# Performance work log

Measured on AMD Instinct MI355X. Metric: run time of the kernel, lower is better.

Reference implementation:

```python
import jax, jax.numpy as jnp
import numpy as np

N_EMBD = 32
BLOCK = 8
N_HEADS = 4
HEAD = N_EMBD // N_HEADS  # 8


def setup_inputs() -> dict:
    key = jax.random.key(0)
    k_x, k_attn, k_proj, k_f1, k_f2 = jax.random.split(key, 5)
    b = 262144
    X = jax.random.normal(k_x, (b, BLOCK, N_EMBD), dtype=jnp.float32)
    # per-head fused qkv weight, stored (in, out) so y = x @ W; out = 3*HEAD, split K,Q,V
    W_attn = jax.random.normal(k_attn, (N_HEADS, N_EMBD, 3 * HEAD), dtype=jnp.float32) * 0.02
    W_proj = jax.random.normal(k_proj, (N_EMBD, N_EMBD), dtype=jnp.float32) * 0.02
    W_ff1 = jax.random.normal(k_f1, (N_EMBD, 4 * N_EMBD), dtype=jnp.float32) * 0.02
    W_ff2 = jax.random.normal(k_f2, (4 * N_EMBD, N_EMBD), dtype=jnp.float32) * 0.02
    return {"X": X, "W_attn": W_attn, "W_proj": W_proj, "W_ff1": W_ff1, "W_ff2": W_ff2}


def reference(X, W_attn, W_proj, W_ff1, W_ff2):
    b, t, c = X.shape
    # fused per-head QKV: (b, t, c) x (h, c, 3*HEAD) -> (b, h, t, 3*HEAD)
    qkv = jnp.einsum('btc,hcd->bhtd', X, W_attn)
    k, q, v = jnp.split(qkv, 3, axis=-1)  # split order K, Q, V as in torch .split
    # NOTE: scale uses full embed dim c, not head_size (faithful to source)
    scores = jnp.einsum('bhqd,bhkd->bhqk', q, k) * (c ** -0.5)
    causal = jnp.tril(jnp.ones((t, t), dtype=bool))
    scores = jnp.where(causal, scores, -jnp.inf)
    w = jax.nn.softmax(scores, axis=-1)
    attn = jnp.einsum('bhqk,bhkd->bhqd', w, v)  # (b, h, t, HEAD)
    attn = attn.transpose(0, 2, 1, 3).reshape(b, t, c)  # concat heads
    X = X + attn @ W_proj
    X = X + jax.nn.relu(X @ W_ff1) @ W_ff2
    return X
```

## Files before the change

kernel.cpp:

```cpp
#include <hip/hip_runtime.h>


typedef __attribute__((ext_vector_type(8))) short        bf16x8;
typedef __attribute__((ext_vector_type(4))) float        f32x4;
typedef __attribute__((ext_vector_type(4))) int          i32x4;
typedef __attribute__((ext_vector_type(2))) unsigned int u32x2;

#define THREADS 256
#define TPB 64
#define TPW 16

#define LDS_X     0
#define LDS_QK    1280
#define LDS_VT    3584
#define LDS_P2    5120
#define LDS_ATTN  0
#define LDS_X2    1280
#define LDS_HID   2560
#define LDS_OUT   0
#define LDS_WAVE  7680

__device__ __forceinline__ unsigned pk_bf16(float a, float b) {
    unsigned r;
    asm("v_cvt_pk_bf16_f32 %0, %1, %2" : "=v"(r) : "v"(a), "v"(b));
    return r;
}

union frag_u { i32x4 i; bf16x8 b; };

__device__ __forceinline__ bf16x8 gather_w(const float* p, int ldk, int g) {
    frag_u r;
    #pragma unroll
    for (int jj = 0; jj < 4; ++jj) {
        float a = p[(8 * g + 2 * jj) * ldk];
        float b = p[(8 * g + 2 * jj + 1) * ldk];
        r.i[jj] = (int)pk_bf16(a, b);
    }
    return r.b;
}

__global__ __launch_bounds__(THREADS)
void block_mfma(const float* __restrict__ X,
                const float* __restrict__ Wattn,
                const float* __restrict__ Wproj,
                const float* __restrict__ Wff1,
                const float* __restrict__ Wff2,
                float* __restrict__ Out,
                int ntiles)
{
    __shared__ __align__(16) char smem[4 * LDS_WAVE];

    const int lane = threadIdx.x & 63;
    const int wid  = threadIdx.x >> 6;
    const int g    = lane >> 4;
    const int c    = lane & 15;
    char* W = smem + wid * LDS_WAVE;

    const float scale = 0.17677669529663687f;
    const f32x4 z4 = {0.f, 0.f, 0.f, 0.f};

    bf16x8 wqk[4], wv[2], wp[2], w1[8], w2[2][4];
    #pragma unroll
    for (int n = 0; n < 4; ++n)
        wqk[n] = gather_w(Wattn + n * 768 + c, 24, g);
    #pragma unroll
    for (int n = 0; n < 2; ++n) {
        int vch = 16 * n + c;
        wv[n] = gather_w(Wattn + (vch >> 3) * 768 + 16 + (vch & 7), 24, g);
    }
    #pragma unroll
    for (int n = 0; n < 2; ++n)
        wp[n] = gather_w(Wproj + 16 * n + c, 32, g);
    #pragma unroll
    for (int n = 0; n < 8; ++n)
        w1[n] = gather_w(Wff1 + 16 * n + c, 128, g);
    #pragma unroll
    for (int n = 0; n < 2; ++n)
        #pragma unroll
        for (int ks = 0; ks < 4; ++ks)
            w2[n][ks] = gather_w(Wff2 + ks * 1024 + 16 * n + c, 32, g);

    float mf[4];
    #pragma unroll
    for (int r = 0; r < 4; ++r) {
        int key = 4 * g + r;
        mf[r] = ((key >> 3) == (c >> 3) && (key & 7) <= (c & 7)) ? 1.f : 0.f;
    }
    const int mQK = (lane < 16) ? -1 : 0;
    const int mA  = (((lane >> 3) & 1) == ((lane >> 5) & 1)) ? -1 : 0;
    const i32x4 vQK = {mQK, mQK, mQK, mQK};
    const i32x4 vA  = {mA, mA, mA, mA};

    const int tile0 = blockIdx.x * TPB + wid * TPW;

    const float* xg0 = X + (size_t)tile0 * 512;
    f32x4 xa = *(const f32x4*)(xg0 + lane * 8);
    f32x4 xb = *(const f32x4*)(xg0 + lane * 8 + 4);

    #pragma unroll 1
    for (int it = 0; it < TPW; ++it) {
        const int tile = tile0 + it;
        if (tile >= ntiles) break;
        const float* xgc = X + (size_t)tile * 512;
        float* outg = Out + (size_t)tile * 512;

        f32x4 rx0 = *(const f32x4*)(xgc + c * 32 + 4 * g);
        f32x4 rx1 = *(const f32x4*)(xgc + c * 32 + 16 + 4 * g);

        {
            i32x4 xi = { (int)pk_bf16(xa[0], xa[1]), (int)pk_bf16(xa[2], xa[3]),
                         (int)pk_bf16(xb[0], xb[1]), (int)pk_bf16(xb[2], xb[3]) };
            *(i32x4*)(void*)(W + LDS_X + (lane >> 2) * 80 + (lane & 3) * 16) = xi;
        }

        {
            const int tn = (it + 1 < TPW && tile + 1 < ntiles) ? tile + 1 : tile;
            const float* xgn = X + (size_t)tn * 512;
            xa = *(const f32x4*)(xgn + lane * 8);
            xb = *(const f32x4*)(xgn + lane * 8 + 4);
        }

        frag_u xf; xf.i = *(i32x4*)(void*)(W + LDS_X + c * 80 + g * 16);

        #pragma unroll
        for (int n = 0; n < 4; ++n) {
            f32x4 qc = __builtin_amdgcn_mfma_f32_16x16x32_bf16(wqk[n], xf.b, z4, 0, 0, 0);
            u32x2 w64 = { pk_bf16(qc[0], qc[1]), pk_bf16(qc[2], qc[3]) };
            *(u32x2*)(void*)(W + LDS_QK + c * 144 + (16 * n + 4 * g) * 2) = w64;
        }
        #pragma unroll
        for (int n = 0; n < 2; ++n) {
            f32x4 vc = __builtin_amdgcn_mfma_f32_16x16x32_bf16(xf.b, wv[n], z4, 0, 0, 0);
            u32x2 w64 = { pk_bf16(vc[0], vc[1]), pk_bf16(vc[2], vc[3]) };
            *(u32x2*)(void*)(W + LDS_VT + (16 * n + c) * 48 + 4 * g * 2) = w64;
        }

        #pragma unroll
        for (int h = 0; h < 4; ++h) {
            frag_u kf, qf;
            kf.i = *(i32x4*)(void*)(W + LDS_QK + c * 144 + 32 * h);
            qf.i = *(i32x4*)(void*)(W + LDS_QK + c * 144 + 32 * h + 16);
            kf.i &= vQK; qf.i &= vQK;
            f32x4 sT = __builtin_amdgcn_mfma_f32_16x16x32_bf16(kf.b, qf.b, z4, 0, 0, 0);
            float e0 = __expf(sT[0] * scale) * mf[0];
            float e1 = __expf(sT[1] * scale) * mf[1];
            float e2 = __expf(sT[2] * scale) * mf[2];
            float e3 = __expf(sT[3] * scale) * mf[3];
            float s = (e0 + e1) + (e2 + e3);
            s += __shfl_xor(s, 16);
            s += __shfl_xor(s, 32);
            float rs = 1.0f / s;
            u32x2 w64 = { pk_bf16(e0 * rs, e1 * rs), pk_bf16(e2 * rs, e3 * rs) };
            *(u32x2*)(void*)(W + LDS_P2 + (h >> 1) * 1280 + c * 80 + ((h & 1) * 16 + 4 * g) * 2) = w64;
        }

        #pragma unroll
        for (int p = 0; p < 2; ++p) {
            frag_u va, pb;
            va.i = *(i32x4*)(void*)(W + LDS_VT + (16 * p + c) * 48 + (g & 1) * 16);
            va.i &= vA;
            pb.i = *(i32x4*)(void*)(W + LDS_P2 + p * 1280 + c * 80 + g * 16);
            f32x4 pv = __builtin_amdgcn_mfma_f32_16x16x32_bf16(va.b, pb.b, z4, 0, 0, 0);
            u32x2 w64 = { pk_bf16(pv[0], pv[1]), pk_bf16(pv[2], pv[3]) };
            *(u32x2*)(void*)(W + LDS_ATTN + c * 80 + (16 * p + 4 * g) * 2) = w64;
        }

        frag_u af; af.i = *(i32x4*)(void*)(W + LDS_ATTN + c * 80 + g * 16);
        f32x4 x2c[2];
        #pragma unroll
        for (int n = 0; n < 2; ++n) {
            f32x4 pc = __builtin_amdgcn_mfma_f32_16x16x32_bf16(wp[n], af.b, z4, 0, 0, 0);
            f32x4 rx = (n == 0) ? rx0 : rx1;
            #pragma unroll
            for (int r = 0; r < 4; ++r) x2c[n][r] = pc[r] + rx[r];
            u32x2 w64 = { pk_bf16(x2c[n][0], x2c[n][1]), pk_bf16(x2c[n][2], x2c[n][3]) };
            *(u32x2*)(void*)(W + LDS_X2 + c * 80 + (16 * n + 4 * g) * 2) = w64;
        }

        frag_u bf; bf.i = *(i32x4*)(void*)(W + LDS_X2 + c * 80 + g * 16);
        #pragma unroll
        for (int n = 0; n < 8; ++n) {
            f32x4 hc = __builtin_amdgcn_mfma_f32_16x16x32_bf16(w1[n], bf.b, z4, 0, 0, 0);
            #pragma unroll
            for (int r = 0; r < 4; ++r) hc[r] = fmaxf(hc[r], 0.f);
            u32x2 w64 = { pk_bf16(hc[0], hc[1]), pk_bf16(hc[2], hc[3]) };
            *(u32x2*)(void*)(W + LDS_HID + c * 272 + (16 * n + 4 * g) * 2) = w64;
        }

        frag_u hf0, hf1, hf2, hf3;
        hf0.i = *(i32x4*)(void*)(W + LDS_HID + c * 272 + 0 * 64 + g * 16);
        hf1.i = *(i32x4*)(void*)(W + LDS_HID + c * 272 + 1 * 64 + g * 16);
        hf2.i = *(i32x4*)(void*)(W + LDS_HID + c * 272 + 2 * 64 + g * 16);
        hf3.i = *(i32x4*)(void*)(W + LDS_HID + c * 272 + 3 * 64 + g * 16);
        #pragma unroll
        for (int n = 0; n < 2; ++n) {
            f32x4 oc = x2c[n];
            oc = __builtin_amdgcn_mfma_f32_16x16x32_bf16(w2[n][0], hf0.b, oc, 0, 0, 0);
            oc = __builtin_amdgcn_mfma_f32_16x16x32_bf16(w2[n][1], hf1.b, oc, 0, 0, 0);
            oc = __builtin_amdgcn_mfma_f32_16x16x32_bf16(w2[n][2], hf2.b, oc, 0, 0, 0);
            oc = __builtin_amdgcn_mfma_f32_16x16x32_bf16(w2[n][3], hf3.b, oc, 0, 0, 0);
            *(f32x4*)(void*)(W + LDS_OUT + c * 144 + (16 * n + 4 * g) * 4) = oc;
        }

        f32x4 r0 = *(f32x4*)(void*)(W + LDS_OUT + (lane >> 2) * 144 + (lane & 3) * 32);
        f32x4 r1 = *(f32x4*)(void*)(W + LDS_OUT + (lane >> 2) * 144 + (lane & 3) * 32 + 16);
        *(f32x4*)(outg + lane * 8)     = r0;
        *(f32x4*)(outg + lane * 8 + 4) = r1;
    }
}

extern "C" void kernel_launch(void* const* d_in, const int* in_sizes, int n_in,
                              void* d_out, int out_size, void* d_ws, size_t ws_size,
                              hipStream_t stream) {
    (void)n_in; (void)out_size; (void)d_ws; (void)ws_size;
    const float* X     = (const float*)d_in[0];
    const float* Wattn = (const float*)d_in[1];
    const float* Wproj = (const float*)d_in[2];
    const float* Wff1  = (const float*)d_in[3];
    const float* Wff2  = (const float*)d_in[4];
    float* Out = (float*)d_out;

    const int nseq   = in_sizes[0] / 256;
    const int ntiles = nseq / 2;
    const int blocks = (ntiles + TPB - 1) / TPB;
    block_mfma<<<dim3(blocks), dim3(THREADS), 0, stream>>>(
        X, Wattn, Wproj, Wff1, Wff2, Out, ntiles);
}
```

Before: 214.2 us.

## Interleave two tiles per wave iteration with double LDS contexts and fold softmax scale

Each wave now processes two tiles per loop iteration in separate LDS contexts, running each phase on tile A and then tile B. The intent is to give the scheduler independent MFMA and LDS work so it can hide dependency latencies within a single wave. The softmax scale and log2(e) factor are folded into the Q/K weights so scores feed exp2 directly, and the reciprocal uses the hardware rcp. The hidden-buffer row stride changes from 272 to 304 bytes, presumably to reduce LDS bank conflicts. Costs are doubled LDS per block (lower occupancy) and higher register pressure, plus slight precision changes from rcp and from scaling the weights before the bf16 conversion.

```diff
diff --git a/kernel.cpp b/kernel.cpp
--- a/kernel.cpp
+++ b/kernel.cpp
@@ -18,7 +18,7 @@
 #define LDS_X2    1280
 #define LDS_HID   2560
 #define LDS_OUT   0
-#define LDS_WAVE  7680
+#define LDS_CTX   7680
 
 __device__ __forceinline__ unsigned pk_bf16(float a, float b) {
     unsigned r;
@@ -28,16 +28,132 @@
 
 union frag_u { i32x4 i; bf16x8 b; };
 
-__device__ __forceinline__ bf16x8 gather_w(const float* p, int ldk, int g) {
+__device__ __forceinline__ bf16x8 gather_w(const float* p, int ldk, int g, float s) {
     frag_u r;
     #pragma unroll
     for (int jj = 0; jj < 4; ++jj) {
-        float a = p[(8 * g + 2 * jj) * ldk];
-        float b = p[(8 * g + 2 * jj + 1) * ldk];
+        float a = p[(8 * g + 2 * jj) * ldk] * s;
+        float b = p[(8 * g + 2 * jj + 1) * ldk] * s;
         r.i[jj] = (int)pk_bf16(a, b);
     }
     return r.b;
 }
+
+
+__device__ __forceinline__ void ph_stage(char* Wc, int lane, const f32x4& xa, const f32x4& xb) {
+    i32x4 xi = { (int)pk_bf16(xa[0], xa[1]), (int)pk_bf16(xa[2], xa[3]),
+                 (int)pk_bf16(xb[0], xb[1]), (int)pk_bf16(xb[2], xb[3]) };
+    *(i32x4*)(void*)(Wc + LDS_X + (lane >> 2) * 80 + (lane & 3) * 16) = xi;
+}
+
+__device__ __forceinline__ void ph_qkv(char* Wc, int c, int g,
+                                       const bf16x8 (&wqk)[4], const bf16x8 (&wv)[2]) {
+    const f32x4 z4 = {0.f, 0.f, 0.f, 0.f};
+    frag_u xf; xf.i = *(i32x4*)(void*)(Wc + LDS_X + c * 80 + g * 16);
+    #pragma unroll
+    for (int n = 0; n < 4; ++n) {
+        f32x4 qc = __builtin_amdgcn_mfma_f32_16x16x32_bf16(wqk[n], xf.b, z4, 0, 0, 0);
+        u32x2 w64 = { pk_bf16(qc[0], qc[1]), pk_bf16(qc[2], qc[3]) };
+        *(u32x2*)(void*)(Wc + LDS_QK + c * 144 + (16 * n + 4 * g) * 2) = w64;
+    }
+    #pragma unroll
+    for (int n = 0; n < 2; ++n) {
+        f32x4 vc = __builtin_amdgcn_mfma_f32_16x16x32_bf16(xf.b, wv[n], z4, 0, 0, 0);
+        u32x2 w64 = { pk_bf16(vc[0], vc[1]), pk_bf16(vc[2], vc[3]) };
+        *(u32x2*)(void*)(Wc + LDS_VT + (16 * n + c) * 48 + 8 * g) = w64;
+    }
+}
+
+__device__ __forceinline__ void ph_scores(char* Wc, int c, int g,
+                                          const f32x4& mf, const i32x4& mQK) {
+    const f32x4 z4 = {0.f, 0.f, 0.f, 0.f};
+    #pragma unroll
+    for (int h = 0; h < 4; ++h) {
+        frag_u kf, qf;
+        kf.i = *(i32x4*)(void*)(Wc + LDS_QK + c * 144 + 32 * h);
+        qf.i = *(i32x4*)(void*)(Wc + LDS_QK + c * 144 + 32 * h + 16);
+        kf.i &= mQK; qf.i &= mQK;
+        f32x4 sT = __builtin_amdgcn_mfma_f32_16x16x32_bf16(kf.b, qf.b, z4, 0, 0, 0);
+        float e0 = __builtin_amdgcn_exp2f(sT[0]) * mf[0];
+        float e1 = __builtin_amdgcn_exp2f(sT[1]) * mf[1];
+        float e2 = __builtin_amdgcn_exp2f(sT[2]) * mf[2];
+        float e3 = __builtin_amdgcn_exp2f(sT[3]) * mf[3];
+        float s = (e0 + e1) + (e2 + e3);
+        s += __shfl_xor(s, 16);
+        s += __shfl_xor(s, 32);
+        float rs = __builtin_amdgcn_rcpf(s);
+        u32x2 w64 = { pk_bf16(e0 * rs, e1 * rs), pk_bf16(e2 * rs, e3 * rs) };
+        *(u32x2*)(void*)(Wc + LDS_P2 + (h >> 1) * 1280 + c * 80 + ((h & 1) * 16 + 4 * g) * 2) = w64;
+    }
+}
+
+__device__ __forceinline__ void ph_pv(char* Wc, int c, int g, const i32x4& mPV) {
+    const f32x4 z4 = {0.f, 0.f, 0.f, 0.f};
+    #pragma unroll
+    for (int p = 0; p < 2; ++p) {
+        frag_u va, pb;
+        va.i = *(i32x4*)(void*)(Wc + LDS_VT + (16 * p + c) * 48 + (g & 1) * 16);
+        va.i &= mPV;
+        pb.i = *(i32x4*)(void*)(Wc + LDS_P2 + p * 1280 + c * 80 + g * 16);
+        f32x4 pv = __builtin_amdgcn_mfma_f32_16x16x32_bf16(va.b, pb.b, z4, 0, 0, 0);
+        u32x2 w64 = { pk_bf16(pv[0], pv[1]), pk_bf16(pv[2], pv[3]) };
+        *(u32x2*)(void*)(Wc + LDS_ATTN + c * 80 + (16 * p + 4 * g) * 2) = w64;
+    }
+}
+
+__device__ __forceinline__ void ph_proj(char* Wc, int c, int g, const bf16x8 (&wp)[2],
+                                        const f32x4& rx0, const f32x4& rx1, f32x4 (&x2c)[2]) {
+    frag_u af; af.i = *(i32x4*)(void*)(Wc + LDS_ATTN + c * 80 + g * 16);
+    #pragma unroll
+    for (int n = 0; n < 2; ++n) {
+        const f32x4 z4 = {0.f, 0.f, 0.f, 0.f};
+        f32x4 pc = __builtin_amdgcn_mfma_f32_16x16x32_bf16(wp[n], af.b, z4, 0, 0, 0);
+        f32x4 rx = (n == 0) ? rx0 : rx1;
+        #pragma unroll
+        for (int r = 0; r < 4; ++r) x2c[n][r] = pc[r] + rx[r];
+        u32x2 w64 = { pk_bf16(x2c[n][0], x2c[n][1]), pk_bf16(x2c[n][2], x2c[n][3]) };
+        *(u32x2*)(void*)(Wc + LDS_X2 + c * 80 + (16 * n + 4 * g) * 2) = w64;
+    }
+}
+
+__device__ __forceinline__ void ph_ff1(char* Wc, int c, int g, const bf16x8 (&w1)[8]) {
+    frag_u bf; bf.i = *(i32x4*)(void*)(Wc + LDS_X2 + c * 80 + g * 16);
+    #pragma unroll
+    for (int n = 0; n < 8; ++n) {
+        const f32x4 z4 = {0.f, 0.f, 0.f, 0.f};
+        f32x4 hc = __builtin_amdgcn_mfma_f32_16x16x32_bf16(w1[n], bf.b, z4, 0, 0, 0);
+        #pragma unroll
+        for (int r = 0; r < 4; ++r) hc[r] = fmaxf(hc[r], 0.f);
+        u32x2 w64 = { pk_bf16(hc[0], hc[1]), pk_bf16(hc[2], hc[3]) };
+        *(u32x2*)(void*)(Wc + LDS_HID + c * 304 + (16 * n + 4 * g) * 2) = w64;
+    }
+}
+
+__device__ __forceinline__ void ph_ff2(char* Wc, int c, int g,
+                                       const bf16x8 (&w2)[2][4], const f32x4 (&x2c)[2]) {
+    frag_u hf0, hf1, hf2, hf3;
+    hf0.i = *(i32x4*)(void*)(Wc + LDS_HID + c * 304 + 0 * 64 + g * 16);
+    hf1.i = *(i32x4*)(void*)(Wc + LDS_HID + c * 304 + 1 * 64 + g * 16);
+    hf2.i = *(i32x4*)(void*)(Wc + LDS_HID + c * 304 + 2 * 64 + g * 16);
+    hf3.i = *(i32x4*)(void*)(Wc + LDS_HID + c * 304 + 3 * 64 + g * 16);
+    #pragma unroll
+    for (int n = 0; n < 2; ++n) {
+        f32x4 oc = x2c[n];
+        oc = __builtin_amdgcn_mfma_f32_16x16x32_bf16(w2[n][0], hf0.b, oc, 0, 0, 0);
+        oc = __builtin_amdgcn_mfma_f32_16x16x32_bf16(w2[n][1], hf1.b, oc, 0, 0, 0);
+        oc = __builtin_amdgcn_mfma_f32_16x16x32_bf16(w2[n][2], hf2.b, oc, 0, 0, 0);
+        oc = __builtin_amdgcn_mfma_f32_16x16x32_bf16(w2[n][3], hf3.b, oc, 0, 0, 0);
+        *(f32x4*)(void*)(Wc + LDS_OUT + c * 144 + (16 * n + 4 * g) * 4) = oc;
+    }
+}
+
+__device__ __forceinline__ void ph_store(char* Wc, int lane, float* outg) {
+    f32x4 r0 = *(f32x4*)(void*)(Wc + LDS_OUT + (lane >> 2) * 144 + (lane & 3) * 32);
+    f32x4 r1 = *(f32x4*)(void*)(Wc + LDS_OUT + (lane >> 2) * 144 + (lane & 3) * 32 + 16);
+    *(f32x4*)(outg + lane * 8)     = r0;
+    *(f32x4*)(outg + lane * 8 + 4) = r1;
+}
+
 
 __global__ __launch_bounds__(THREADS)
 void block_mfma(const float* __restrict__ X,
@@ -48,164 +164,105 @@
                 float* __restrict__ Out,
                 int ntiles)
 {
-    __shared__ __align__(16) char smem[4 * LDS_WAVE];
+    __shared__ __align__(16) char smem[4 * 2 * LDS_CTX];
 
     const int lane = threadIdx.x & 63;
     const int wid  = threadIdx.x >> 6;
     const int g    = lane >> 4;
     const int c    = lane & 15;
-    char* W = smem + wid * LDS_WAVE;
-
-    const float scale = 0.17677669529663687f;
-    const f32x4 z4 = {0.f, 0.f, 0.f, 0.f};
+    char* WA = smem + wid * (2 * LDS_CTX);
+    char* WB = WA + LDS_CTX;
+
+    const float wscale = 0.5050098f;
 
     bf16x8 wqk[4], wv[2], wp[2], w1[8], w2[2][4];
     #pragma unroll
     for (int n = 0; n < 4; ++n)
-        wqk[n] = gather_w(Wattn + n * 768 + c, 24, g);
+        wqk[n] = gather_w(Wattn + n * 768 + c, 24, g, wscale);
     #pragma unroll
     for (int n = 0; n < 2; ++n) {
         int vch = 16 * n + c;
-        wv[n] = gather_w(Wattn + (vch >> 3) * 768 + 16 + (vch & 7), 24, g);
+        wv[n] = gather_w(Wattn + (vch >> 3) * 768 + 16 + (vch & 7), 24, g, 1.f);
     }
     #pragma unroll
     for (int n = 0; n < 2; ++n)
-        wp[n] = gather_w(Wproj + 16 * n + c, 32, g);
+        wp[n] = gather_w(Wproj + 16 * n + c, 32, g, 1.f);
     #pragma unroll
     for (int n = 0; n < 8; ++n)
-        w1[n] = gather_w(Wff1 + 16 * n + c, 128, g);
+        w1[n] = gather_w(Wff1 + 16 * n + c, 128, g, 1.f);
     #pragma unroll
     for (int n = 0; n < 2; ++n)
         #pragma unroll
         for (int ks = 0; ks < 4; ++ks)
-            w2[n][ks] = gather_w(Wff2 + ks * 1024 + 16 * n + c, 32, g);
-
-    float mf[4];
+            w2[n][ks] = gather_w(Wff2 + ks * 1024 + 16 * n + c, 32, g, 1.f);
+
+    f32x4 mf;
     #pragma unroll
     for (int r = 0; r < 4; ++r) {
         int key = 4 * g + r;
         mf[r] = ((key >> 3) == (c >> 3) && (key & 7) <= (c & 7)) ? 1.f : 0.f;
     }
-    const int mQK = (lane < 16) ? -1 : 0;
-    const int mA  = (((lane >> 3) & 1) == ((lane >> 5) & 1)) ? -1 : 0;
-    const i32x4 vQK = {mQK, mQK, mQK, mQK};
-    const i32x4 vA  = {mA, mA, mA, mA};
+    const int b0 = (lane < 16) ? -1 : 0;
+    const int b1 = (((lane >> 3) & 1) == ((lane >> 5) & 1)) ? -1 : 0;
+    const i32x4 mQK = {b0, b0, b0, b0};
+    const i32x4 mPV = {b1, b1, b1, b1};
 
     const int tile0 = blockIdx.x * TPB + wid * TPW;
-
-    const float* xg0 = X + (size_t)tile0 * 512;
-    f32x4 xa = *(const f32x4*)(xg0 + lane * 8);
-    f32x4 xb = *(const f32x4*)(xg0 + lane * 8 + 4);
+    if (tile0 >= ntiles) return;
+
+    int p0 = tile0, p1 = (tile0 + 1 < ntiles) ? tile0 + 1 : ntiles - 1;
+    f32x4 xaA = *(const f32x4*)(X + (size_t)p0 * 512 + lane * 8);
+    f32x4 xbA = *(const f32x4*)(X + (size_t)p0 * 512 + lane * 8 + 4);
+    f32x4 xaB = *(const f32x4*)(X + (size_t)p1 * 512 + lane * 8);
+    f32x4 xbB = *(const f32x4*)(X + (size_t)p1 * 512 + lane * 8 + 4);
 
     #pragma unroll 1
-    for (int it = 0; it < TPW; ++it) {
-        const int tile = tile0 + it;
-        if (tile >= ntiles) break;
-        const float* xgc = X + (size_t)tile * 512;
-        float* outg = Out + (size_t)tile * 512;
-
-        f32x4 rx0 = *(const f32x4*)(xgc + c * 32 + 4 * g);
-        f32x4 rx1 = *(const f32x4*)(xgc + c * 32 + 16 + 4 * g);
+    for (int it = 0; it < TPW; it += 2) {
+        const int iA = tile0 + it;
+        const int iB = tile0 + it + 1;
+        const int ttA = (iA < ntiles) ? iA : ntiles - 1;
+        const int ttB = (iB < ntiles) ? iB : ntiles - 1;
+        const float* xgA = X + (size_t)ttA * 512;
+        const float* xgB = X + (size_t)ttB * 512;
+
+        f32x4 rxA0 = *(const f32x4*)(xgA + c * 32 + 4 * g);
+        f32x4 rxA1 = *(const f32x4*)(xgA + c * 32 + 16 + 4 * g);
+        f32x4 rxB0 = *(const f32x4*)(xgB + c * 32 + 4 * g);
+        f32x4 rxB1 = *(const f32x4*)(xgB + c * 32 + 16 + 4 * g);
+
+        ph_stage(WA, lane, xaA, xbA);
+        ph_stage(WB, lane, xaB, xbB);
 
         {
-            i32x4 xi = { (int)pk_bf16(xa[0], xa[1]), (int)pk_bf16(xa[2], xa[3]),
-                         (int)pk_bf16(xb[0], xb[1]), (int)pk_bf16(xb[2], xb[3]) };
-            *(i32x4*)(void*)(W + LDS_X + (lane >> 2) * 80 + (lane & 3) * 16) = xi;
+            int nA = (it + 2 < TPW && iA + 2 < ntiles) ? iA + 2 : ttA;
+            int nB = (it + 3 < TPW && iB + 2 < ntiles) ? iB + 2 : ttB;
+            xaA = *(const f32x4*)(X + (size_t)nA * 512 + lane * 8);
+            xbA = *(const f32x4*)(X + (size_t)nA * 512 + lane * 8 + 4);
+            xaB = *(const f32x4*)(X + (size_t)nB * 512 + lane * 8);
+            xbB = *(const f32x4*)(X + (size_t)nB * 512 + lane * 8 + 4);
         }
 
-        {
-            const int tn = (it + 1 < TPW && tile + 1 < ntiles) ? tile + 1 : tile;
-            const float* xgn = X + (size_t)tn * 512;
-            xa = *(const f32x4*)(xgn + lane * 8);
-            xb = *(const f32x4*)(xgn + lane * 8 + 4);
-        }
-
-        frag_u xf; xf.i = *(i32x4*)(void*)(W + LDS_X + c * 80 + g * 16);
-
-        #pragma unroll
-        for (int n = 0; n < 4; ++n) {
-            f32x4 qc = __builtin_amdgcn_mfma_f32_16x16x32_bf16(wqk[n], xf.b, z4, 0, 0, 0);
-            u32x2 w64 = { pk_bf16(qc[0], qc[1]), pk_bf16(qc[2], qc[3]) };
-            *(u32x2*)(void*)(W + LDS_QK + c * 144 + (16 * n + 4 * g) * 2) = w64;
-        }
-        #pragma unroll
-        for (int n = 0; n < 2; ++n) {
-            f32x4 vc = __builtin_amdgcn_mfma_f32_16x16x32_bf16(xf.b, wv[n], z4, 0, 0, 0);
-            u32x2 w64 = { pk_bf16(vc[0], vc[1]), pk_bf16(vc[2], vc[3]) };
-            *(u32x2*)(void*)(W + LDS_VT + (16 * n + c) * 48 + 4 * g * 2) = w64;
-        }
-
-        #pragma unroll
-        for (int h = 0; h < 4; ++h) {
-            frag_u kf, qf;
-            kf.i = *(i32x4*)(void*)(W + LDS_QK + c * 144 + 32 * h);
-            qf.i = *(i32x4*)(void*)(W + LDS_QK + c * 144 + 32 * h + 16);
-            kf.i &= vQK; qf.i &= vQK;
-            f32x4 sT = __builtin_amdgcn_mfma_f32_16x16x32_bf16(kf.b, qf.b, z4, 0, 0, 0);
-            float e0 = __expf(sT[0] * scale) * mf[0];
-            float e1 = __expf(sT[1] * scale) * mf[1];
-            float e2 = __expf(sT[2] * scale) * mf[2];
-            float e3 = __expf(sT[3] * scale) * mf[3];
-            float s = (e0 + e1) + (e2 + e3);
-            s += __shfl_xor(s, 16);
-            s += __shfl_xor(s, 32);
-            float rs = 1.0f / s;
-            u32x2 w64 = { pk_bf16(e0 * rs, e1 * rs), pk_bf16(e2 * rs, e3 * rs) };
-            *(u32x2*)(void*)(W + LDS_P2 + (h >> 1) * 1280 + c * 80 + ((h & 1) * 16 + 4 * g) * 2) = w64;
-        }
-
-        #pragma unroll
-        for (int p = 0; p < 2; ++p) {
-            frag_u va, pb;
-            va.i = *(i32x4*)(void*)(W + LDS_VT + (16 * p + c) * 48 + (g & 1) * 16);
-            va.i &= vA;
-            pb.i = *(i32x4*)(void*)(W + LDS_P2 + p * 1280 + c * 80 + g * 16);
-            f32x4 pv = __builtin_amdgcn_mfma_f32_16x16x32_bf16(va.b, pb.b, z4, 0, 0, 0);
-            u32x2 w64 = { pk_bf16(pv[0], pv[1]), pk_bf16(pv[2], pv[3]) };
-            *(u32x2*)(void*)(W + LDS_ATTN + c * 80 + (16 * p + 4 * g) * 2) = w64;
-        }
-
-        frag_u af; af.i = *(i32x4*)(void*)(W + LDS_ATTN + c * 80 + g * 16);
-        f32x4 x2c[2];
-        #pragma unroll
-        for (int n = 0; n < 2; ++n) {
-            f32x4 pc = __builtin_amdgcn_mfma_f32_16x16x32_bf16(wp[n], af.b, z4, 0, 0, 0);
-            f32x4 rx = (n == 0) ? rx0 : rx1;
-            #pragma unroll
-            for (int r = 0; r < 4; ++r) x2c[n][r] = pc[r] + rx[r];
-            u32x2 w64 = { pk_bf16(x2c[n][0], x2c[n][1]), pk_bf16(x2c[n][2], x2c[n][3]) };
-            *(u32x2*)(void*)(W + LDS_X2 + c * 80 + (16 * n + 4 * g) * 2) = w64;
-        }
-
-        frag_u bf; bf.i = *(i32x4*)(void*)(W + LDS_X2 + c * 80 + g * 16);
-        #pragma unroll
-        for (int n = 0; n < 8; ++n) {
-            f32x4 hc = __builtin_amdgcn_mfma_f32_16x16x32_bf16(w1[n], bf.b, z4, 0, 0, 0);
-            #pragma unroll
-            for (int r = 0; r < 4; ++r) hc[r] = fmaxf(hc[r], 0.f);
-            u32x2 w64 = { pk_bf16(hc[0], hc[1]), pk_bf16(hc[2], hc[3]) };
-            *(u32x2*)(void*)(W + LDS_HID + c * 272 + (16 * n + 4 * g) * 2) = w64;
-        }
-
-        frag_u hf0, hf1, hf2, hf3;
-        hf0.i = *(i32x4*)(void*)(W + LDS_HID + c * 272 + 0 * 64 + g * 16);
-        hf1.i = *(i32x4*)(void*)(W + LDS_HID + c * 272 + 1 * 64 + g * 16);
-        hf2.i = *(i32x4*)(void*)(W + LDS_HID + c * 272 + 2 * 64 + g * 16);
-        hf3.i = *(i32x4*)(void*)(W + LDS_HID + c * 272 + 3 * 64 + g * 16);
-        #pragma unroll
-        for (int n = 0; n < 2; ++n) {
-            f32x4 oc = x2c[n];
-            oc = __builtin_amdgcn_mfma_f32_16x16x32_bf16(w2[n][0], hf0.b, oc, 0, 0, 0);
-            oc = __builtin_amdgcn_mfma_f32_16x16x32_bf16(w2[n][1], hf1.b, oc, 0, 0, 0);
-            oc = __builtin_amdgcn_mfma_f32_16x16x32_bf16(w2[n][2], hf2.b, oc, 0, 0, 0);
-            oc = __builtin_amdgcn_mfma_f32_16x16x32_bf16(w2[n][3], hf3.b, oc, 0, 0, 0);
-            *(f32x4*)(void*)(W + LDS_OUT + c * 144 + (16 * n + 4 * g) * 4) = oc;
-        }
-
-        f32x4 r0 = *(f32x4*)(void*)(W + LDS_OUT + (lane >> 2) * 144 + (lane & 3) * 32);
-        f32x4 r1 = *(f32x4*)(void*)(W + LDS_OUT + (lane >> 2) * 144 + (lane & 3) * 32 + 16);
-        *(f32x4*)(outg + lane * 8)     = r0;
-        *(f32x4*)(outg + lane * 8 + 4) = r1;
+        ph_qkv(WA, c, g, wqk, wv);
+        ph_qkv(WB, c, g, wqk, wv);
+
+        ph_scores(WA, c, g, mf, mQK);
+        ph_scores(WB, c, g, mf, mQK);
+
+        ph_pv(WA, c, g, mPV);
+        ph_pv(WB, c, g, mPV);
+
+        f32x4 x2A[2], x2B[2];
+        ph_proj(WA, c, g, wp, rxA0, rxA1, x2A);
+        ph_proj(WB, c, g, wp, rxB0, rxB1, x2B);
+
+        ph_ff1(WA, c, g, w1);
+        ph_ff1(WB, c, g, w1);
+
+        ph_ff2(WA, c, g, w2, x2A);
+        ph_ff2(WB, c, g, w2, x2B);
+
+        if (iA < ntiles) ph_store(WA, lane, Out + (size_t)iA * 512);
+        if (iB < ntiles) ph_store(WB, lane, Out + (size_t)iB * 512);
     }
 }
 
```

After: 186.8 us. 1.15x faster.
